# Kernel optimization log

Hardware: AMD Instinct MI355X
Metric: run time of the kernel (lower is better)

Reference implementation:

```python
import jax, jax.numpy as jnp
import numpy as np
from jax import lax

B, FCH, H, W = 2, 48, 512, 512
WNUM, PATCH = 1, 8
DEG = 180.0 / np.pi
# well-conditioned, slightly asymmetric fallback Mueller matrix for masked (non-physical) pixels
_SAFE = np.array([[1.0, 0.02, 0.01, 0.005],
                  [0.0, 0.95, 0.05, 0.0],
                  [0.0, -0.05, 0.90, 0.04],
                  [0.0, 0.0, -0.04, 0.85]], dtype=np.float32)


def setup_inputs():
    key = jax.random.key(0)
    x = 0.5 * jax.random.normal(key, (B, FCH, H, W), dtype=jnp.float32)
    eye = jnp.eye(4, dtype=jnp.float32).reshape(16)
    # bias intensity frames and both calibration matrices toward 2*I so per-pixel
    # 4x4 systems are well conditioned and M is near-physical
    boost = jnp.concatenate([2.0 * eye, 2.0 * eye, 2.0 * eye])[None, :, None, None]
    return {"x": x + boost}


def _charpoly_mask(M):
    # Cloude realizability test: characteristic-polynomial coefficients of the
    # Hermitian coherency matrix must all be >= 0 (all eigenvalues >= 0).
    s = jnp.stack([jnp.eye(2, dtype=jnp.complex64),
                   jnp.array([[1, 0], [0, -1]], jnp.complex64),
                   jnp.array([[0, 1], [1, 0]], jnp.complex64),
                   jnp.array([[0, -1j], [1j, 0]], jnp.complex64)])
    Bk = jnp.einsum('iab,jcd->ijacbd', s, s).reshape(16, 4, 4)  # kron(sigma_i, sigma_j)
    Hc = 0.25 * jnp.einsum('...k,kab->...ab', M.reshape(M.shape[:-2] + (16,)).astype(jnp.complex64), Bk)
    tr1 = jnp.trace(Hc, axis1=-2, axis2=-1).real
    H2 = Hc @ Hc
    tr2 = jnp.trace(H2, axis1=-2, axis2=-1).real
    tr3 = jnp.trace(H2 @ Hc, axis1=-2, axis2=-1).real
    c2 = 0.5 * (tr1 ** 2 - tr2)
    c3 = (tr1 ** 3 - 3.0 * tr1 * tr2 + 2.0 * tr3) / 6.0
    c4 = jnp.linalg.det(Hc).real
    return (tr1 >= 0) & (c2 >= 0) & (c3 >= 0) & (c4 >= 0)


def _compute_mm(A, F, Wm, norm=True):
    M = jnp.linalg.solve(A, F)  # A^-1 F
    M = jnp.swapaxes(jnp.linalg.solve(jnp.swapaxes(Wm, -1, -2), jnp.swapaxes(M, -1, -2)), -1, -2)  # ... W^-1
    return M / M[..., 0:1, 0:1] if norm else M


def _lu_chipman(M, mask):
    # Lu-Chipman polar decomposition M = M_delta @ M_R @ M_D (per pixel)
    M = jnp.where(mask[..., None, None], M, jnp.asarray(_SAFE))
    I3 = jnp.eye(3, dtype=M.dtype)
    D = M[..., 0, 1:]  # diattenuation vector
    d2 = jnp.clip(jnp.sum(D * D, -1), 0.0, 1.0 - 1e-6)
    d = jnp.sqrt(d2 + 1e-12)
    sq = jnp.sqrt(1.0 - d2)
    Dh = D / jnp.maximum(d, 1e-6)[..., None]
    mD = sq[..., None, None] * I3 + (1.0 - sq)[..., None, None] * (Dh[..., :, None] * Dh[..., None, :])
    ones = jnp.ones(M.shape[:-2] + (1,), M.dtype)
    MD = jnp.concatenate([jnp.concatenate([ones, D], -1)[..., None, :],
                          jnp.concatenate([D[..., None], mD], -1)], -2)
    Mp = jnp.swapaxes(jnp.linalg.solve(MD, jnp.swapaxes(M, -1, -2)), -1, -2)  # M @ MD^-1 (MD symmetric)
    mp = Mp[..., 1:, 1:]
    mm = mp @ jnp.swapaxes(mp, -1, -2)
    lam = jnp.clip(jnp.linalg.eigvalsh(mm), 1e-12, None)  # ascending
    s1, s2, s3 = jnp.sqrt(lam[..., 2]), jnp.sqrt(lam[..., 1]), jnp.sqrt(lam[..., 0])
    sgn = jnp.where(jnp.linalg.det(mp) < 0, -1.0, 1.0).astype(M.dtype)
    A3 = mm + (s1 * s2 + s2 * s3 + s3 * s1)[..., None, None] * I3 + 1e-6 * I3
    B3 = (s1 + s2 + s3)[..., None, None] * mm + (s1 * s2 * s3)[..., None, None] * I3
    mdel = sgn[..., None, None] * jnp.linalg.solve(A3, B3)
    Pdel = (M[..., 1:, 0] - jnp.einsum('...ij,...j->...i', M[..., 1:, 1:], D)) / (1.0 - d2)[..., None]
    top = jnp.concatenate([ones, jnp.zeros(M.shape[:-2] + (3,), M.dtype)], -1)[..., None, :]
    Mdel = jnp.concatenate([top, jnp.concatenate([Pdel[..., None], mdel], -1)], -2)
    MR = jnp.linalg.solve(Mdel + 1e-6 * jnp.eye(4, dtype=M.dtype), Mp)
    return MD, MR, Mdel


def _polarimetry(MD, MR, Mdel):
    clipc = lambda t: jnp.clip(t, -1.0 + 1e-6, 1.0 - 1e-6)
    D = MD[..., 0, 1:]
    totD = jnp.sqrt(jnp.sum(D * D, -1) + 1e-12)
    linD = jnp.sqrt(D[..., 0] ** 2 + D[..., 1] ** 2 + 1e-12)
    cirD = jnp.abs(D[..., 2])
    totR = jnp.arccos(clipc(jnp.trace(MR, axis1=-2, axis2=-1) / 2.0 - 1.0)) * DEG
    mR = MR[..., 1:, 1:]
    linR = jnp.arccos(clipc(jnp.sqrt((mR[..., 0, 0] + mR[..., 1, 1]) ** 2
                                     + (mR[..., 1, 0] - mR[..., 0, 1]) ** 2 + 1e-12) - 1.0)) * DEG
    cirR = 0.5 * jnp.arctan2(mR[..., 1, 0] - mR[..., 0, 1], mR[..., 0, 0] + mR[..., 1, 1]) * DEG
    # azimuth of linear retardance from retardance-vector components (r1, r2)
    azi = jnp.mod(0.5 * jnp.arctan2(mR[..., 2, 0] - mR[..., 0, 2], mR[..., 1, 2] - mR[..., 2, 1]) * DEG, 180.0)
    dazi = jnp.mod(0.5 * jnp.arctan2(D[..., 1], D[..., 0]) * DEG, 180.0)
    totP = 1.0 - jnp.abs(jnp.trace(Mdel[..., 1:, 1:], axis1=-2, axis2=-1)) / 3.0
    # p[:,0]=diattenuation, p[:,6]=linear retardance, p[:,7]=azimuth, p[:,-1]=depolarization
    return jnp.stack([totD, linD, cirD, totR, cirR, dazi, linR, azi, totP], axis=1)


def _rolling_circstd(a_deg, patch):
    # circstd(a/180*pi, high=pi, low=0) over patch x patch sliding windows, back to degrees.
    # circstd reduces to window means of cos/sin of doubled angles -> avg pooling.
    th = a_deg * (2.0 * np.pi / 180.0)
    wsum = lambda t: lax.reduce_window(t, 0.0, lax.add, (1, 1, patch, patch), (1, 1, 1, 1), 'SAME')
    cnt = wsum(jnp.ones_like(a_deg))
    R = jnp.sqrt(wsum(jnp.cos(th)) ** 2 + wsum(jnp.sin(th)) ** 2 + 1e-12) / cnt
    R = jnp.clip(R, 1e-7, 1.0 - 1e-7)
    return 0.5 * jnp.sqrt(-2.0 * jnp.log(R)) * DEG


def _forward(x):
    b, f, h, w = x.shape
    xw = jnp.moveaxis(x.reshape(b, WNUM, f // WNUM, h, w), 2, -1)  # (b, wnum, h, w, 48)
    Fi = xw[..., :16].reshape(b, WNUM, h, w, 4, 4)
    Am = xw[..., 16:32].reshape(b, WNUM, h, w, 4, 4)
    Wm = xw[..., 32:48].reshape(b, WNUM, h, w, 4, 4)
    M = _compute_mm(Am, Fi, Wm, norm=True)
    inten = xw[..., 0]
    imin = inten.min(axis=(1, 2, 3), keepdims=True)
    imax = inten.max(axis=(1, 2, 3), keepdims=True)
    inorm = (inten - imin) / (imax - imin)
    mchan = jnp.moveaxis(M.reshape(b, WNUM, h, w, 16), -1, 2).reshape(b, WNUM * 16, h, w)
    v = lax.stop_gradient(_charpoly_mask(M))
    MD, MR, Mdel = _lu_chipman(M, v)
    p = _polarimetry(MD, MR, Mdel)  # (b, 9, wnum, h, w)
    std = _rolling_circstd(p[:, 7], PATCH)
    # concat order matches forward: intensity, mueller, linr, totp, datt, azimuth, std
    return jnp.concatenate([inorm, mchan, p[:, 6], p[:, 8], p[:, 0], p[:, 7], std], axis=1)


def reference(x):
    return _forward(x)
```

## Files before the change

kernel.cpp:

```cpp
#include <hip/hip_runtime.h>
#include <math.h>

#define B_ 2
#define H_ 512
#define W_ 512
#define HW_ (H_ * W_)
#define NCH_IN 48
#define NCH_OUT 22
#define DEG_ 57.29577951308232f

__device__ __forceinline__ float frcp(float x)  { return __builtin_amdgcn_rcpf(x); }
__device__ __forceinline__ float frcp_nr(float x) {
    float r = __builtin_amdgcn_rcpf(x);
    return r * __builtin_fmaf(-x, r, 2.0f);
}
__device__ __forceinline__ float fsqrtf_(float x){ return __builtin_amdgcn_sqrtf(x); }

__device__ __forceinline__ float fast_acos(float x) {
    float ax = fabsf(x);
    float t = fsqrtf_(fmaxf(1.0f - ax, 0.0f));
    float p = t * (1.5707288f + ax * (-0.2121144f + ax * (0.0742610f + ax * (-0.0187293f))));
    return (x >= 0.0f) ? p : (3.14159265358979f - p);
}

__device__ __forceinline__ float fast_atan2(float y, float x) {
    float ay = fabsf(y), ax = fabsf(x);
    float mx = fmaxf(ax, ay), mn = fminf(ax, ay);
    float a = mn * frcp(fmaxf(mx, 1e-37f));
    float s = a * a;
    float r = a * (0.99997726f + s * (-0.33262347f + s * (0.19354346f +
              s * (-0.11643287f + s * (0.05265332f + s * (-0.01172120f))))));
    if (ay > ax) r = 1.57079632679f - r;
    if (x < 0.0f) r = 3.14159265359f - r;
    return (y < 0.0f) ? -r : r;
}

__device__ __forceinline__ unsigned int fkey(float f) {
    unsigned int u = __float_as_uint(f);
    return (u & 0x80000000u) ? ~u : (u | 0x80000000u);
}
__device__ __forceinline__ float funkey(unsigned int k) {
    return (k & 0x80000000u) ? __uint_as_float(k ^ 0x80000000u) : __uint_as_float(~k);
}

__global__ __launch_bounds__(256) void minmax_kernel(const float* __restrict__ x,
                                                     unsigned int* __restrict__ mm) {
    int b = blockIdx.x >> 6;
    int blk = blockIdx.x & 63;
    const float* src = x + (size_t)b * NCH_IN * HW_;
    float lo = INFINITY, hi = -INFINITY;
    for (int i = blk * 256 + threadIdx.x; i < HW_; i += 64 * 256) {
        float v = src[i];
        lo = fminf(lo, v);
        hi = fmaxf(hi, v);
    }
    __shared__ float slo[256], shi[256];
    slo[threadIdx.x] = lo; shi[threadIdx.x] = hi;
    __syncthreads();
    for (int s = 128; s > 0; s >>= 1) {
        if (threadIdx.x < s) {
            slo[threadIdx.x] = fminf(slo[threadIdx.x], slo[threadIdx.x + s]);
            shi[threadIdx.x] = fmaxf(shi[threadIdx.x], shi[threadIdx.x + s]);
        }
        __syncthreads();
    }
    if (threadIdx.x == 0) {
        atomicMax(&mm[2 * b], ~fkey(slo[0]));
        atomicMax(&mm[2 * b + 1], fkey(shi[0]));
    }
}

__device__ __forceinline__ void solve4(const float A[4][4], const float Bm[4][4], float X[4][4]) {
    float m[4][8];
#pragma unroll
    for (int i = 0; i < 4; i++) {
#pragma unroll
        for (int j = 0; j < 4; j++) { m[i][j] = A[i][j]; m[i][j + 4] = Bm[i][j]; }
    }
#pragma unroll
    for (int k = 0; k < 4; k++) {
#pragma unroll
        for (int r = k + 1; r < 4; r++) {
            bool sw = fabsf(m[r][k]) > fabsf(m[k][k]);
#pragma unroll
            for (int c = 0; c < 8; c++) {
                float a = m[k][c], b = m[r][c];
                m[k][c] = sw ? b : a;
                m[r][c] = sw ? a : b;
            }
        }
        float piv = frcp_nr(m[k][k]);
#pragma unroll
        for (int c = 0; c < 8; c++) m[k][c] *= piv;
#pragma unroll
        for (int r = 0; r < 4; r++) {
            if (r == k) continue;
            float f = m[r][k];
#pragma unroll
            for (int c = 0; c < 8; c++) m[r][c] -= f * m[k][c];
        }
    }
#pragma unroll
    for (int i = 0; i < 4; i++)
#pragma unroll
        for (int j = 0; j < 4; j++) X[i][j] = m[i][j + 4];
}

__device__ __forceinline__ void mul4(const float A[4][4], const float B[4][4], float C[4][4]) {
#pragma unroll
    for (int i = 0; i < 4; i++)
#pragma unroll
        for (int j = 0; j < 4; j++) {
            float s = 0.0f;
#pragma unroll
            for (int k = 0; k < 4; k++) s += A[i][k] * B[k][j];
            C[i][j] = s;
        }
}

__device__ __forceinline__ void inv3(const float A[3][3], float out[3][3]) {
    float c00 = A[1][1] * A[2][2] - A[1][2] * A[2][1];
    float c01 = A[1][2] * A[2][0] - A[1][0] * A[2][2];
    float c02 = A[1][0] * A[2][1] - A[1][1] * A[2][0];
    float det = A[0][0] * c00 + A[0][1] * c01 + A[0][2] * c02;
    float id = frcp_nr(det);
    out[0][0] = c00 * id;
    out[0][1] = (A[0][2] * A[2][1] - A[0][1] * A[2][2]) * id;
    out[0][2] = (A[0][1] * A[1][2] - A[0][2] * A[1][1]) * id;
    out[1][0] = c01 * id;
    out[1][1] = (A[0][0] * A[2][2] - A[0][2] * A[2][0]) * id;
    out[1][2] = (A[0][2] * A[1][0] - A[0][0] * A[1][2]) * id;
    out[2][0] = c02 * id;
    out[2][1] = (A[0][1] * A[2][0] - A[0][0] * A[2][1]) * id;
    out[2][2] = (A[0][0] * A[1][1] - A[0][1] * A[1][0]) * id;
}

__device__ __forceinline__ float det3(const float A[3][3]) {
    return A[0][0] * (A[1][1] * A[2][2] - A[1][2] * A[2][1])
         - A[0][1] * (A[1][0] * A[2][2] - A[1][2] * A[2][0])
         + A[0][2] * (A[1][0] * A[2][1] - A[1][1] * A[2][0]);
}

__device__ __forceinline__ void eig3_sym(const float A[3][3], float& l1, float& l2, float& l3) {
    float q = (A[0][0] + A[1][1] + A[2][2]) * (1.0f / 3.0f);
    float a00 = A[0][0] - q, a11 = A[1][1] - q, a22 = A[2][2] - q;
    float off = A[0][1] * A[0][1] + A[0][2] * A[0][2] + A[1][2] * A[1][2];
    float p2 = a00 * a00 + a11 * a11 + a22 * a22 + 2.0f * off;
    float p = fsqrtf_(p2 * (1.0f / 6.0f) + 1e-30f);
    float inv = frcp(p);
    float b00 = a00 * inv, b11 = a11 * inv, b22 = a22 * inv;
    float b01 = A[0][1] * inv, b02 = A[0][2] * inv, b12 = A[1][2] * inv;
    float detB = b00 * (b11 * b22 - b12 * b12)
               - b01 * (b01 * b22 - b12 * b02)
               + b02 * (b01 * b12 - b11 * b02);
    float r = 0.5f * detB;
    r = fminf(fmaxf(r, -1.0f), 1.0f);
    float phi = fast_acos(r) * (1.0f / 3.0f);
    l1 = q + 2.0f * p * __cosf(phi);
    l3 = q + 2.0f * p * __cosf(phi + 2.0943951023931953f);
    l2 = 3.0f * q - l1 - l3;
}

__global__ __launch_bounds__(256) void main_kernel(const float* __restrict__ x,
                                                   const unsigned int* __restrict__ mmk,
                                                   float* __restrict__ out) {
    int idx = blockIdx.x * 256 + threadIdx.x;
    if (idx >= B_ * HW_) return;
    int b = idx / HW_;
    int p = idx - b * HW_;
    const float* src = x + (size_t)b * NCH_IN * HW_ + p;

    float F[4][4], A[4][4], WT[4][4];
#pragma unroll
    for (int i = 0; i < 4; i++)
#pragma unroll
        for (int j = 0; j < 4; j++) {
            F[i][j]  = __builtin_nontemporal_load(&src[(4 * i + j) * HW_]);
            A[i][j]  = __builtin_nontemporal_load(&src[(16 + 4 * i + j) * HW_]);
            WT[j][i] = __builtin_nontemporal_load(&src[(32 + 4 * i + j) * HW_]);
        }
    float inten = F[0][0];

    float X[4][4], XT[4][4], MT[4][4], M[4][4];
    solve4(A, F, X);
#pragma unroll
    for (int i = 0; i < 4; i++)
#pragma unroll
        for (int j = 0; j < 4; j++) XT[i][j] = X[j][i];
    solve4(WT, XT, MT);
    float nrm = frcp_nr(MT[0][0]);
#pragma unroll
    for (int i = 0; i < 4; i++)
#pragma unroll
        for (int j = 0; j < 4; j++) M[i][j] = MT[j][i] * nrm;

    float* ob = out + (size_t)b * NCH_OUT * HW_ + p;
    float imin = funkey(~mmk[2 * b]), imax = funkey(mmk[2 * b + 1]);
    __builtin_nontemporal_store((inten - imin) * frcp(imax - imin), &ob[0]);
#pragma unroll
    for (int k = 0; k < 16; k++)
        __builtin_nontemporal_store(M[k >> 2][k & 3], &ob[(size_t)(1 + k) * HW_]);

    {
        float a0 = M[0][0], b0 = M[0][1], c0 = M[0][2], e0 = M[0][3];
        float a1 = M[1][0], b1 = M[1][1], c1 = M[1][2], e1 = M[1][3];
        float a2 = M[2][0], b2 = M[2][1], c2_ = M[2][2], e2 = M[2][3];
        float a3 = M[3][0], b3 = M[3][1], c3_ = M[3][2], e3 = M[3][3];
        float sa = a0 + a1, da = a0 - a1, sb = b0 + b1, db = b0 - b1;
        float d0 = sa + sb, d1 = sa - sb, d2 = da + db, d3 = da - db;
        float u01r = c0 + c1,  u01i = -(e0 + e1);
        float u23r = c0 - c1,  u23i = -(e0 - e1);
        float u02r = a2 + b2,  u02i = -(a3 + b3);
        float u13r = a2 - b2,  u13i = -(a3 - b3);
        float u03r = c2_ - e3, u03i = -(e2 + c3_);
        float u12r = c2_ + e3, u12i =  (e2 - c3_);

        float n01 = u01r * u01r + u01i * u01i;
        float n02 = u02r * u02r + u02i * u02i;
        float n03 = u03r * u03r + u03i * u03i;
        float n12 = u12r * u12r + u12i * u12i;
        float n13 = u13r * u13r + u13i * u13i;
        float n23 = u23r * u23r + u23i * u23i;

        float q0 = d0 * d0 + n01 + n02 + n03;
        float q1 = d1 * d1 + n01 + n12 + n13;
        float q2 = d2 * d2 + n02 + n12 + n23;
        float q3 = d3 * d3 + n03 + n13 + n23;
        float p2 = q0 + q1 + q2 + q3;

        float w01r = (d0 + d1) * u01r + (u02r * u12r + u02i * u12i) + (u03r * u13r + u03i * u13i);
        float w01i = (d0 + d1) * u01i + (u02i * u12r - u02r * u12i) + (u03i * u13r - u03r * u13i);
        float w02r = (d0 + d2) * u02r + (u01r * u12r - u01i * u12i) + (u03r * u23r + u03i * u23i);
        float w02i = (d0 + d2) * u02i + (u01r * u12i + u01i * u12r) + (u03i * u23r - u03r * u23i);
        float w03r = (d0 + d3) * u03r + (u01r * u13r - u01i * u13i) + (u02r * u23r - u02i * u23i);
        float w03i = (d0 + d3) * u03i + (u01r * u13i + u01i * u13r) + (u02r * u23i + u02i * u23r);
        float w12r = (d1 + d2) * u12r + (u01r * u02r + u01i * u02i) + (u13r * u23r + u13i * u23i);
        float w12i = (d1 + d2) * u12i + (u01r * u02i - u01i * u02r) + (u13i * u23r - u13r * u23i);
        float w13r = (d1 + d3) * u13r + (u01r * u03r + u01i * u03i) + (u12r * u23r - u12i * u23i);
        float w13i = (d1 + d3) * u13i + (u01r * u03i - u01i * u03r) + (u12r * u23i + u12i * u23r);
        float w23r = (d2 + d3) * u23r + (u02r * u03r + u02i * u03i) + (u12r * u13r + u12i * u13i);
        float w23i = (d2 + d3) * u23i + (u02r * u03i - u02i * u03r) + (u12i * u13r - u12r * u13i);

        float p3 = q0 * d0 + q1 * d1 + q2 * d2 + q3 * d3
                 + 2.0f * (w01r * u01r + w01i * u01i + w02r * u02r + w02i * u02i
                         + w03r * u03r + w03i * u03i + w12r * u12r + w12i * u12i
                         + w13r * u13r + w13i * u13i + w23r * u23r + w23i * u23i);
        float p4 = q0 * q0 + q1 * q1 + q2 * q2 + q3 * q3
                 + 2.0f * (w01r * w01r + w01i * w01i + w02r * w02r + w02i * w02i
                         + w03r * w03r + w03i * w03i + w12r * w12r + w12i * w12i
                         + w13r * w13r + w13i * w13i + w23r * w23r + w23i * w23i);

        float tr1 = 4.0f * a0;
        float t2 = tr1 * tr1;
        float c2v = t2 - p2;
        float c3v = tr1 * t2 - 3.0f * tr1 * p2 + 2.0f * p3;
        float c4v = t2 * t2 - 6.0f * t2 * p2 + 3.0f * p2 * p2 + 8.0f * tr1 * p3 - 6.0f * p4;
        bool mask = (tr1 >= 0.0f) && (c2v >= 0.0f) && (c3v >= 0.0f) && (c4v >= 0.0f);

        const float SAFE[4][4] = {{1.0f, 0.02f, 0.01f, 0.005f},
                                  {0.0f, 0.95f, 0.05f, 0.0f},
                                  {0.0f, -0.05f, 0.9f, 0.04f},
                                  {0.0f, 0.0f, -0.04f, 0.85f}};
#pragma unroll
        for (int i = 0; i < 4; i++)
#pragma unroll
            for (int j = 0; j < 4; j++) M[i][j] = mask ? M[i][j] : SAFE[i][j];
    }

    float D0 = M[0][1], D1 = M[0][2], D2v = M[0][3];
    float d2r = D0 * D0 + D1 * D1 + D2v * D2v;
    float totD = fsqrtf_(d2r + 1e-12f);
    float d2 = fminf(fmaxf(d2r, 0.0f), 1.0f - 1e-6f);
    float d = fsqrtf_(d2 + 1e-12f);
    float sq2 = 1.0f - d2;
    float sq = fsqrtf_(sq2);
    float dinv = frcp(fmaxf(d, 1e-6f));
    float h0 = D0 * dinv, h1 = D1 * dinv, h2 = D2v * dinv;

    float isq2 = frcp_nr(sq2);
    float isq = frcp(sq);
    float cdh = (1.0f - sq) * isq2;
    float MDi[4][4];
    MDi[0][0] = isq2;
    MDi[0][1] = -isq2 * D0; MDi[0][2] = -isq2 * D1; MDi[0][3] = -isq2 * D2v;
    MDi[1][0] = MDi[0][1];  MDi[2][0] = MDi[0][2];  MDi[3][0] = MDi[0][3];
    float Dh[3] = {h0, h1, h2};
#pragma unroll
    for (int i = 0; i < 3; i++)
#pragma unroll
        for (int j = 0; j < 3; j++)
            MDi[1 + i][1 + j] = ((i == j) ? isq : 0.0f) + cdh * Dh[i] * Dh[j];

    float Mp[4][4];
    mul4(M, MDi, Mp);

    float mp3[3][3];
#pragma unroll
    for (int i = 0; i < 3; i++)
#pragma unroll
        for (int j = 0; j < 3; j++) mp3[i][j] = Mp[1 + i][1 + j];
    float mmS[3][3];
#pragma unroll
    for (int i = 0; i < 3; i++)
#pragma unroll
        for (int j = 0; j < 3; j++) {
            float s = 0.0f;
#pragma unroll
            for (int k = 0; k < 3; k++) s += mp3[i][k] * mp3[j][k];
            mmS[i][j] = s;
        }
    float l1, l2, l3;
    eig3_sym(mmS, l1, l2, l3);
    l1 = fmaxf(l1, 1e-12f); l2 = fmaxf(l2, 1e-12f); l3 = fmaxf(l3, 1e-12f);
    float s1 = fsqrtf_(l1), s2 = fsqrtf_(l2), s3 = fsqrtf_(l3);
    float sgn = (det3(mp3) < 0.0f) ? -1.0f : 1.0f;

    float e2s = s1 * s2 + s2 * s3 + s3 * s1 + 1e-6f;
    float e1s = s1 + s2 + s3;
    float e3s = s1 * s2 * s3;
    float A3[3][3], B3[3][3];
#pragma unroll
    for (int i = 0; i < 3; i++)
#pragma unroll
        for (int j = 0; j < 3; j++) {
            A3[i][j] = mmS[i][j] + ((i == j) ? e2s : 0.0f);
            B3[i][j] = e1s * mmS[i][j] + ((i == j) ? e3s : 0.0f);
        }
    float A3i[3][3];
    inv3(A3, A3i);
    float mdel[3][3];
#pragma unroll
    for (int i = 0; i < 3; i++)
#pragma unroll
        for (int j = 0; j < 3; j++) {
            float s = 0.0f;
#pragma unroll
            for (int k = 0; k < 3; k++) s += A3i[i][k] * B3[k][j];
            mdel[i][j] = sgn * s;
        }

    float Pd[3];
#pragma unroll
    for (int i = 0; i < 3; i++)
        Pd[i] = (M[1 + i][0] - (M[1 + i][1] * D0 + M[1 + i][2] * D1 + M[1 + i][3] * D2v)) * isq2;

    float MR0[4];
    const float inv_aeps = 1.0f / (1.0f + 1e-6f);
#pragma unroll
    for (int j = 0; j < 4; j++) MR0[j] = Mp[0][j] * inv_aeps;
    float m3[3][3];
#pragma unroll
    for (int i = 0; i < 3; i++)
#pragma unroll
        for (int j = 0; j < 3; j++) m3[i][j] = mdel[i][j] + ((i == j) ? 1e-6f : 0.0f);
    float m3i[3][3];
    inv3(m3, m3i);
    float MRr[3][4];
#pragma unroll
    for (int i = 0; i < 3; i++)
#pragma unroll
        for (int j = 0; j < 4; j++) {
            float s = 0.0f;
#pragma unroll
            for (int k = 0; k < 3; k++) s += m3i[i][k] * (Mp[1 + k][j] - Pd[k] * MR0[j]);
            MRr[i][j] = s;
        }

    float mR00 = MRr[0][1], mR01 = MRr[0][2], mR02 = MRr[0][3];
    float mR10 = MRr[1][1], mR11 = MRr[1][2], mR12 = MRr[1][3];
    float mR20 = MRr[2][1], mR21 = MRr[2][2];

    float t_lin = fsqrtf_((mR00 + mR11) * (mR00 + mR11) + (mR10 - mR01) * (mR10 - mR01) + 1e-12f) - 1.0f;
    t_lin = fminf(fmaxf(t_lin, -1.0f + 1e-6f), 1.0f - 1e-6f);
    float linR = fast_acos(t_lin) * DEG_;

    float azi = 0.5f * fast_atan2(mR20 - mR02, mR12 - mR21) * DEG_;
    if (azi < 0.0f) azi += 180.0f;

    float totP = 1.0f - fabsf(mdel[0][0] + mdel[1][1] + mdel[2][2]) * (1.0f / 3.0f);

    __builtin_nontemporal_store(linR, &ob[(size_t)17 * HW_]);
    __builtin_nontemporal_store(totP, &ob[(size_t)18 * HW_]);
    __builtin_nontemporal_store(totD, &ob[(size_t)19 * HW_]);
    ob[(size_t)20 * HW_] = azi;
}

#define TX_ 32
#define TY_ 8
__global__ __launch_bounds__(256) void circstd_kernel(float* __restrict__ out) {
    int tx0 = blockIdx.x * TX_;
    int ty0 = blockIdx.y * TY_;
    int b = blockIdx.z;
    const float* azi = out + (size_t)b * NCH_OUT * HW_ + (size_t)20 * HW_;

    __shared__ float lc[TY_ + 7][TX_ + 8];
    __shared__ float ls[TY_ + 7][TX_ + 8];
    __shared__ float hc[TY_ + 7][TX_];
    __shared__ float hs[TY_ + 7][TX_];

    for (int i = threadIdx.x; i < (TY_ + 7) * (TX_ + 7); i += 256) {
        int row = i / (TX_ + 7);
        int col = i - row * (TX_ + 7);
        int gy = ty0 - 3 + row;
        int gx = tx0 - 3 + col;
        float c = 0.0f, s = 0.0f;
        if (gy >= 0 && gy < H_ && gx >= 0 && gx < W_) {
            float th = azi[(size_t)gy * W_ + gx] * 0.03490658503988659f;
            __sincosf(th, &s, &c);
        }
        lc[row][col] = c; ls[row][col] = s;
    }
    __syncthreads();

    for (int i = threadIdx.x; i < (TY_ + 7) * TX_; i += 256) {
        int row = i / TX_;
        int col = i - row * TX_;
        float sc = 0.0f, ss = 0.0f;
#pragma unroll
        for (int d = 0; d < 8; d++) { sc += lc[row][col + d]; ss += ls[row][col + d]; }
        hc[row][col] = sc; hs[row][col] = ss;
    }
    __syncthreads();

    int col = threadIdx.x & (TX_ - 1);
    int row = threadIdx.x >> 5;
    float sc = 0.0f, ss = 0.0f;
#pragma unroll
    for (int k = 0; k < 8; k++) { sc += hc[row + k][col]; ss += hs[row + k][col]; }
    int y = ty0 + row, xc = tx0 + col;
    float rows = (float)(min(y + 5, H_) - max(y - 3, 0));
    float cols = (float)(min(xc + 5, W_) - max(xc - 3, 0));
    float R = fsqrtf_(sc * sc + ss * ss + 1e-12f) * frcp(rows * cols);
    R = fminf(fmaxf(R, 1e-7f), 1.0f - 1e-7f);
    float stdv = 0.5f * fsqrtf_(-2.0f * __logf(R)) * DEG_;
    __builtin_nontemporal_store(stdv,
        &out[(size_t)b * NCH_OUT * HW_ + (size_t)21 * HW_ + (size_t)y * W_ + xc]);
}

extern "C" void kernel_launch(void* const* d_in, const int* in_sizes, int n_in,
                              void* d_out, int out_size, void* d_ws, size_t ws_size,
                              hipStream_t stream) {
    const float* x = (const float*)d_in[0];
    float* out = (float*)d_out;
    unsigned int* mmk = (unsigned int*)d_ws;

    hipMemsetAsync(mmk, 0, 4 * sizeof(unsigned int), stream);
    hipLaunchKernelGGL(minmax_kernel, dim3(128), dim3(256), 0, stream, x, mmk);
    hipLaunchKernelGGL(main_kernel, dim3((B_ * HW_ + 255) / 256), dim3(256), 0, stream, x, mmk, out);
    hipLaunchKernelGGL(circstd_kernel, dim3(W_ / TX_, H_ / TY_, B_), dim3(256), 0, stream, out);
}
```

Baseline: 171.3 us.

## Process both batch pixels per thread with interleaved dual 4x4 solves

Each thread now handles the same pixel position for both batch elements, running the two Gauss-Jordan eliminations interleaved to expose instruction-level parallelism, and halving the grid. The elimination also skips columns already reduced and uses explicit FMAs. The per-thread work in the tail doubles, which raises register pressure and may cut occupancy or cause spills.

```diff
diff --git a/kernel.cpp b/kernel.cpp
--- a/kernel.cpp
+++ b/kernel.cpp
@@ -70,40 +70,42 @@
     }
 }
 
-__device__ __forceinline__ void solve4(const float A[4][4], const float Bm[4][4], float X[4][4]) {
-    float m[4][8];
-#pragma unroll
-    for (int i = 0; i < 4; i++) {
-#pragma unroll
-        for (int j = 0; j < 4; j++) { m[i][j] = A[i][j]; m[i][j + 4] = Bm[i][j]; }
-    }
+__device__ __forceinline__ void solve4_dual(float m[2][4][8]) {
 #pragma unroll
     for (int k = 0; k < 4; k++) {
 #pragma unroll
         for (int r = k + 1; r < 4; r++) {
-            bool sw = fabsf(m[r][k]) > fabsf(m[k][k]);
-#pragma unroll
-            for (int c = 0; c < 8; c++) {
-                float a = m[k][c], b = m[r][c];
-                m[k][c] = sw ? b : a;
-                m[r][c] = sw ? a : b;
+#pragma unroll
+            for (int q = 0; q < 2; q++) {
+                bool sw = fabsf(m[q][r][k]) > fabsf(m[q][k][k]);
+#pragma unroll
+                for (int c = k; c < 8; c++) {
+                    float a = m[q][k][c], b = m[q][r][c];
+                    m[q][k][c] = sw ? b : a;
+                    m[q][r][c] = sw ? a : b;
+                }
             }
         }
-        float piv = frcp_nr(m[k][k]);
-#pragma unroll
-        for (int c = 0; c < 8; c++) m[k][c] *= piv;
+        float piv[2];
+#pragma unroll
+        for (int q = 0; q < 2; q++) piv[q] = frcp_nr(m[q][k][k]);
+#pragma unroll
+        for (int c = k + 1; c < 8; c++) {
+#pragma unroll
+            for (int q = 0; q < 2; q++) m[q][k][c] *= piv[q];
+        }
 #pragma unroll
         for (int r = 0; r < 4; r++) {
             if (r == k) continue;
-            float f = m[r][k];
-#pragma unroll
-            for (int c = 0; c < 8; c++) m[r][c] -= f * m[k][c];
-        }
-    }
-#pragma unroll
-    for (int i = 0; i < 4; i++)
-#pragma unroll
-        for (int j = 0; j < 4; j++) X[i][j] = m[i][j + 4];
+#pragma unroll
+            for (int q = 0; q < 2; q++) {
+                float f = m[q][r][k];
+#pragma unroll
+                for (int c = k + 1; c < 8; c++)
+                    m[q][r][c] = __builtin_fmaf(-f, m[q][k][c], m[q][r][c]);
+            }
+        }
+    }
 }
 
 __device__ __forceinline__ void mul4(const float A[4][4], const float B[4][4], float C[4][4]) {
@@ -161,41 +163,8 @@
     l2 = 3.0f * q - l1 - l3;
 }
 
-__global__ __launch_bounds__(256) void main_kernel(const float* __restrict__ x,
-                                                   const unsigned int* __restrict__ mmk,
-                                                   float* __restrict__ out) {
-    int idx = blockIdx.x * 256 + threadIdx.x;
-    if (idx >= B_ * HW_) return;
-    int b = idx / HW_;
-    int p = idx - b * HW_;
-    const float* src = x + (size_t)b * NCH_IN * HW_ + p;
-
-    float F[4][4], A[4][4], WT[4][4];
-#pragma unroll
-    for (int i = 0; i < 4; i++)
-#pragma unroll
-        for (int j = 0; j < 4; j++) {
-            F[i][j]  = __builtin_nontemporal_load(&src[(4 * i + j) * HW_]);
-            A[i][j]  = __builtin_nontemporal_load(&src[(16 + 4 * i + j) * HW_]);
-            WT[j][i] = __builtin_nontemporal_load(&src[(32 + 4 * i + j) * HW_]);
-        }
-    float inten = F[0][0];
-
-    float X[4][4], XT[4][4], MT[4][4], M[4][4];
-    solve4(A, F, X);
-#pragma unroll
-    for (int i = 0; i < 4; i++)
-#pragma unroll
-        for (int j = 0; j < 4; j++) XT[i][j] = X[j][i];
-    solve4(WT, XT, MT);
-    float nrm = frcp_nr(MT[0][0]);
-#pragma unroll
-    for (int i = 0; i < 4; i++)
-#pragma unroll
-        for (int j = 0; j < 4; j++) M[i][j] = MT[j][i] * nrm;
-
-    float* ob = out + (size_t)b * NCH_OUT * HW_ + p;
-    float imin = funkey(~mmk[2 * b]), imax = funkey(mmk[2 * b + 1]);
+__device__ __forceinline__ void pixel_tail(float M[4][4], float inten,
+                                           float imin, float imax, float* ob) {
     __builtin_nontemporal_store((inten - imin) * frcp(imax - imin), &ob[0]);
 #pragma unroll
     for (int k = 0; k < 16; k++)
@@ -385,6 +354,60 @@
     ob[(size_t)20 * HW_] = azi;
 }
 
+__global__ __launch_bounds__(256) void main_kernel(const float* __restrict__ x,
+                                                   const unsigned int* __restrict__ mmk,
+                                                   float* __restrict__ out) {
+    int idx = blockIdx.x * 256 + threadIdx.x;
+
+    float m[2][4][8];
+    float WT[2][4][4];
+    float inten[2];
+#pragma unroll
+    for (int q = 0; q < 2; q++) {
+        const float* src = x + (size_t)q * NCH_IN * HW_ + idx;
+#pragma unroll
+        for (int i = 0; i < 4; i++)
+#pragma unroll
+            for (int j = 0; j < 4; j++) {
+                m[q][i][4 + j] = __builtin_nontemporal_load(&src[(4 * i + j) * HW_]);
+                m[q][i][j]     = __builtin_nontemporal_load(&src[(16 + 4 * i + j) * HW_]);
+                WT[q][j][i]    = __builtin_nontemporal_load(&src[(32 + 4 * i + j) * HW_]);
+            }
+        inten[q] = m[q][0][4];
+    }
+
+    solve4_dual(m);
+
+    float m2[2][4][8];
+#pragma unroll
+    for (int q = 0; q < 2; q++)
+#pragma unroll
+        for (int i = 0; i < 4; i++)
+#pragma unroll
+            for (int j = 0; j < 4; j++) {
+                m2[q][i][j]     = WT[q][i][j];
+                m2[q][i][4 + j] = m[q][j][4 + i];
+            }
+    solve4_dual(m2);
+
+    float M[2][4][4];
+#pragma unroll
+    for (int q = 0; q < 2; q++) {
+        float nrm = frcp_nr(m2[q][0][4]);
+#pragma unroll
+        for (int i = 0; i < 4; i++)
+#pragma unroll
+            for (int j = 0; j < 4; j++) M[q][i][j] = m2[q][j][4 + i] * nrm;
+    }
+
+#pragma unroll
+    for (int q = 0; q < 2; q++) {
+        float* ob = out + (size_t)q * NCH_OUT * HW_ + idx;
+        float imin = funkey(~mmk[2 * q]), imax = funkey(mmk[2 * q + 1]);
+        pixel_tail(M[q], inten[q], imin, imax, ob);
+    }
+}
+
 #define TX_ 32
 #define TY_ 8
 __global__ __launch_bounds__(256) void circstd_kernel(float* __restrict__ out) {
@@ -446,6 +469,6 @@
 
     hipMemsetAsync(mmk, 0, 4 * sizeof(unsigned int), stream);
     hipLaunchKernelGGL(minmax_kernel, dim3(128), dim3(256), 0, stream, x, mmk);
-    hipLaunchKernelGGL(main_kernel, dim3((B_ * HW_ + 255) / 256), dim3(256), 0, stream, x, mmk, out);
+    hipLaunchKernelGGL(main_kernel, dim3(HW_ / 256), dim3(256), 0, stream, x, mmk, out);
     hipLaunchKernelGGL(circstd_kernel, dim3(W_ / TX_, H_ / TY_, B_), dim3(256), 0, stream, out);
 }
```

Result: no change. 171.6 us (+0.2%).
